# Kernel tuning notes

Hardware: AMD Instinct MI355X
Metric: run time of the kernel (lower is better)

The kernel has to match this reference:

```python
import jax, jax.numpy as jnp
import numpy as np

B, C, N = 4, 192, 4096
K = 16                      # avg degree
E = B * N * K               # 262144 edges
C_OUT = 384


def setup_inputs() -> dict:
    key = jax.random.key(0)
    k1, k2, k3, k4 = jax.random.split(key, 4)
    x = jax.random.normal(k1, (B, C, N, 1), dtype=jnp.float32)
    edge_index = jax.random.randint(k2, (2, E), 0, B * N, dtype=jnp.int64)
    # BasicConv([2C, C_OUT]): 1x1 Conv2d + bias + ReLU (norm=None)
    W = jax.random.normal(k3, (C_OUT, 2 * C), dtype=jnp.float32) * (1.0 / np.sqrt(2 * C))
    b = jax.random.normal(k4, (C_OUT,), dtype=jnp.float32) * 0.01
    return {"x": x, "edge_index": edge_index, "W": W, "b": b}


def reference(x, edge_index, W, b):
    Bs, Cs, Ns, _ = x.shape
    BN = Bs * Ns
    # (B,C,N,1) -> flattened node table (B*N, C); node id = b*N + n
    x_flat = jnp.transpose(x[..., 0], (0, 2, 1)).reshape(BN, Cs)
    x_i = x_flat[edge_index[0]]          # (E, C) gather at dst
    x_j = x_flat[edge_index[1]]          # (E, C) gather at src
    diff = x_j - x_i
    # scatter-max over dst nodes; torch_scatter fills empty segments with 0
    agg = jax.ops.segment_max(diff, edge_index[0], num_segments=BN)
    agg = jnp.where(jnp.isfinite(agg), agg, 0.0)
    x_j_out = jnp.transpose(agg.reshape(Bs, Ns, Cs), (0, 2, 1))[..., None]  # (B,C,N,1)
    # interleave channels: cat along new axis 2 then reshape -> (B, 2C, N, 1)
    cat = jnp.stack([x, x_j_out], axis=2).reshape(Bs, 2 * Cs, Ns, 1)
    # 1x1 conv == GEMM over channels, + bias + ReLU
    out = jnp.einsum('oc,bcnw->bonw', W, cat) + b[None, :, None, None]
    return jax.nn.relu(out)
```

## Files before the change

kernel.cpp:

```cpp
#include <hip/hip_runtime.h>
#include <hip/hip_bf16.h>
#include <math.h>

#define Bz    4
#define Cch   192
#define Nn    4096
#define BN    16384
#define Ecnt  262144
#define COUT  384
#define CAP   64

typedef __attribute__((ext_vector_type(8))) short short8;
typedef __attribute__((ext_vector_type(4))) float floatx4;

__device__ __forceinline__ void gload_lds16(const void* g, void* l) {
    __builtin_amdgcn_global_load_lds(
        (const __attribute__((address_space(1))) unsigned int*)g,
        (__attribute__((address_space(3))) unsigned int*)l, 16, 0, 0);
}

__device__ __forceinline__ float b2f(unsigned short u) {
    union { unsigned int i; float f; } z; z.i = ((unsigned int)u) << 16; return z.f;
}
__device__ __forceinline__ unsigned short f2b(float f) {
    __hip_bfloat16 h = __float2bfloat16(f);
    return *(unsigned short*)&h;
}

__global__ __launch_bounds__(256) void prep_kernel(
    const float* __restrict__ x, const unsigned int* __restrict__ ew,
    const float* __restrict__ W, __hip_bfloat16* __restrict__ xb,
    __hip_bfloat16* __restrict__ Wxa, __hip_bfloat16* __restrict__ Wa,
    int* __restrict__ deg, int* __restrict__ flag) {
    int bid = blockIdx.x;
    if (bid < 3072) {
        __shared__ float tile[32][33];
        int b = bid / 768;
        int r = bid - b * 768;
        int c0 = (r >> 7) * 32;
        int n0 = (r & 127) * 32;
        int tx = threadIdx.x & 31, ty = threadIdx.x >> 5;
        for (int i = ty; i < 32; i += 8)
            tile[i][tx] = x[((size_t)(b * Cch + c0 + i)) * Nn + n0 + tx];
        __syncthreads();
        for (int i = ty; i < 32; i += 8)
            xb[((size_t)(b * Nn + n0 + i)) * Cch + c0 + tx] =
                __float2bfloat16(tile[tx][i]);
    } else if (bid < 3360) {
        int i = (bid - 3072) * 256 + threadIdx.x;
        int o = i / Cch, c = i - o * Cch;
        float wx = W[o * 2 * Cch + 2 * c];
        float wa = W[o * 2 * Cch + 2 * c + 1];
        Wxa[i] = __float2bfloat16(wx - wa);
        Wa[i]  = __float2bfloat16(wa);
    } else if (bid < 3424) {
        deg[(bid - 3360) * 256 + threadIdx.x] = 0;
    } else {
        __shared__ int s;
        if (threadIdx.x == 0) s = 1;
        __syncthreads();
        if (ew[2 * threadIdx.x + 1] != 0u) atomicAnd(&s, 0);
        __syncthreads();
        if (threadIdx.x == 0) *flag = s;
    }
}

__global__ __launch_bounds__(256) void fill_kernel(
    const int* __restrict__ ew, const int* __restrict__ flag,
    int* __restrict__ deg, int* __restrict__ slots) {
    int t = blockIdx.x * 256 + threadIdx.x;
    int d0, d1, s0, s1;
    if (*flag) {
        int4 dv = *(const int4*)&ew[4 * t];
        int4 sv = *(const int4*)&ew[2 * Ecnt + 4 * t];
        d0 = dv.x; d1 = dv.z; s0 = sv.x; s1 = sv.z;
    } else {
        int2 dv = *(const int2*)&ew[2 * t];
        int2 sv = *(const int2*)&ew[Ecnt + 2 * t];
        d0 = dv.x; d1 = dv.y; s0 = sv.x; s1 = sv.y;
    }
    int p0 = atomicAdd(&deg[d0], 1); if (p0 < CAP) slots[(d0 << 6) + p0] = s0;
    int p1 = atomicAdd(&deg[d1], 1); if (p1 < CAP) slots[(d1 << 6) + p1] = s1;
}

__global__ __launch_bounds__(256) void agg_kernel(
    const int* __restrict__ deg, const int* __restrict__ slots,
    const __hip_bfloat16* __restrict__ xb, __hip_bfloat16* __restrict__ Mb) {
    int lane = threadIdx.x & 63, wave = threadIdx.x >> 6;
    int node = (blockIdx.x << 2) + wave;
    int d = deg[node]; if (d > CAP) d = CAP;
    int nbrval = 0;
    if (lane < d) nbrval = slots[(node << 6) + lane];
    const unsigned short* xbu = (const unsigned short*)xb;
    int act = lane < 48;
    int cb = lane * 4;
    float m0 = -INFINITY, m1 = -INFINITY, m2 = -INFINITY, m3 = -INFINITY;
    int k = 0;
    for (; k + 4 <= d; k += 4) {
        int s0 = __shfl(nbrval, k);
        int s1 = __shfl(nbrval, k + 1);
        int s2 = __shfl(nbrval, k + 2);
        int s3 = __shfl(nbrval, k + 3);
        if (act) {
            ushort4 v0 = *(const ushort4*)&xbu[s0 * Cch + cb];
            ushort4 v1 = *(const ushort4*)&xbu[s1 * Cch + cb];
            ushort4 v2 = *(const ushort4*)&xbu[s2 * Cch + cb];
            ushort4 v3 = *(const ushort4*)&xbu[s3 * Cch + cb];
            m0 = fmaxf(fmaxf(m0, b2f(v0.x)), fmaxf(fmaxf(b2f(v1.x), b2f(v2.x)), b2f(v3.x)));
            m1 = fmaxf(fmaxf(m1, b2f(v0.y)), fmaxf(fmaxf(b2f(v1.y), b2f(v2.y)), b2f(v3.y)));
            m2 = fmaxf(fmaxf(m2, b2f(v0.z)), fmaxf(fmaxf(b2f(v1.z), b2f(v2.z)), b2f(v3.z)));
            m3 = fmaxf(fmaxf(m3, b2f(v0.w)), fmaxf(fmaxf(b2f(v1.w), b2f(v2.w)), b2f(v3.w)));
        }
    }
    for (; k < d; k++) {
        int s = __shfl(nbrval, k);
        if (act) {
            ushort4 v = *(const ushort4*)&xbu[s * Cch + cb];
            m0 = fmaxf(m0, b2f(v.x)); m1 = fmaxf(m1, b2f(v.y));
            m2 = fmaxf(m2, b2f(v.z)); m3 = fmaxf(m3, b2f(v.w));
        }
    }
    if (act) {
        ushort4 o4;
        if (d > 0) {
            o4.x = f2b(m0); o4.y = f2b(m1); o4.z = f2b(m2); o4.w = f2b(m3);
        } else {
            o4 = *(const ushort4*)&xbu[node * Cch + cb];
        }
        *(ushort4*)&((unsigned short*)Mb)[node * Cch + cb] = o4;
    }
}

__global__ __launch_bounds__(256) void gemm_kernel(
    const __hip_bfloat16* __restrict__ Xb, const __hip_bfloat16* __restrict__ Ab,
    const __hip_bfloat16* __restrict__ Wxa, const __hip_bfloat16* __restrict__ Wa,
    const float* __restrict__ bias, float* __restrict__ out) {
    __shared__ short As[64 * 32];
    __shared__ short Bs[128 * 32];
    int t = threadIdx.x;
    int node0 = blockIdx.x * 64;
    int o0    = blockIdx.y * 128;
    int lane = t & 63, wave = t >> 6;
    int quad = lane >> 4, lrow = lane & 15;
    int wm = wave & 1, wn = wave >> 1;

    floatx4 acc[2][4] = {};
    int srow = t >> 2;
    int koff = (t & 3) * 8;

    const __hip_bfloat16* Asrc[2] = {Xb, Ab};
    const __hip_bfloat16* Bsrc[2] = {Wxa, Wa};

    for (int seg = 0; seg < 2; seg++) {
        const __hip_bfloat16* a_g = Asrc[seg] + (size_t)(node0 + srow) * Cch + koff;
        const __hip_bfloat16* b_g = Bsrc[seg] + (size_t)(o0 + srow) * Cch + koff;
        for (int kt = 0; kt < Cch; kt += 32) {
            __syncthreads();
            gload_lds16(a_g + kt,                    &As[t * 8]);
            gload_lds16(b_g + kt,                    &Bs[t * 8]);
            gload_lds16(b_g + kt + (size_t)64 * Cch, &Bs[2048 + t * 8]);
            __syncthreads();
            short8 af[2], bf[4];
#pragma unroll
            for (int i = 0; i < 2; i++)
                af[i] = *(const short8*)&As[(wm * 32 + i * 16 + lrow) * 32 + quad * 8];
#pragma unroll
            for (int j = 0; j < 4; j++)
                bf[j] = *(const short8*)&Bs[(wn * 64 + j * 16 + lrow) * 32 + quad * 8];
#pragma unroll
            for (int i = 0; i < 2; i++)
#pragma unroll
                for (int j = 0; j < 4; j++)
                    acc[i][j] = __builtin_amdgcn_mfma_f32_16x16x32_bf16(bf[j], af[i], acc[i][j], 0, 0, 0);
        }
    }

#pragma unroll
    for (int i = 0; i < 2; i++) {
        int node = node0 + wm * 32 + i * 16 + lrow;
        int b = node >> 12, n = node & 4095;
#pragma unroll
        for (int j = 0; j < 4; j++) {
            int ob = o0 + wn * 64 + j * 16 + quad * 4;
#pragma unroll
            for (int r = 0; r < 4; r++) {
                int o = ob + r;
                float v = acc[i][j][r] + bias[o];
                out[((size_t)(b * COUT + o)) * Nn + n] = fmaxf(v, 0.0f);
            }
        }
    }
}

extern "C" void kernel_launch(void* const* d_in, const int* in_sizes, int n_in,
                              void* d_out, int out_size, void* d_ws, size_t ws_size,
                              hipStream_t stream) {
    const float* x    = (const float*)d_in[0];
    const int*   ew   = (const int*)d_in[1];
    const float* W    = (const float*)d_in[2];
    const float* bias = (const float*)d_in[3];
    float* out        = (float*)d_out;

    char* ws = (char*)d_ws;
    __hip_bfloat16* xb   = (__hip_bfloat16*)ws;
    __hip_bfloat16* Mb   = (__hip_bfloat16*)(ws + 6291456);
    __hip_bfloat16* Wxa  = (__hip_bfloat16*)(ws + 12582912);
    __hip_bfloat16* Wa   = (__hip_bfloat16*)(ws + 12730368);
    int* deg   = (int*)(ws + 12877824);
    int* slots = (int*)(ws + 12943360);
    int* flag  = (int*)(ws + 17137664);

    prep_kernel<<<3425, 256, 0, stream>>>(x, (const unsigned int*)ew, W, xb, Wxa, Wa, deg, flag);
    fill_kernel<<<Ecnt / 512, 256, 0, stream>>>(ew, flag, deg, slots);
    agg_kernel<<<BN / 4, 256, 0, stream>>>(deg, slots, xb, Mb);
    gemm_kernel<<<dim3(BN / 64, COUT / 128), 256, 0, stream>>>(xb, Mb, Wxa, Wa, bias, out);
}
```

Measured before the change: 117.2 us.

## Double-buffer GEMM LDS tiles and unroll aggregation gather to 8 neighbors

The GEMM kernel now ping-pongs between two LDS buffers, issuing the next K-slab's global-to-LDS loads before computing on the current one, with one barrier per step instead of two. The aggregation kernel makes the degree wave-uniform, uses readlane instead of shuffles for neighbor indices, and processes eight neighbor rows per iteration to put more gathers in flight. The aim is to hide global load latency in both kernels, at the cost of doubled LDS use and more registers. The double-buffer relies on the barrier at the end of each step to keep the buffer being refilled safe from reads still in progress.

```diff
diff --git a/kernel.cpp b/kernel.cpp
--- a/kernel.cpp
+++ b/kernel.cpp
@@ -83,12 +83,20 @@
     int p1 = atomicAdd(&deg[d1], 1); if (p1 < CAP) slots[(d1 << 6) + p1] = s1;
 }
 
+#define RED8(mm, FLD) do {                                                    \
+    float a_ = fmaxf(fmaxf(b2f(v[0].FLD), b2f(v[1].FLD)),                     \
+                     fmaxf(b2f(v[2].FLD), b2f(v[3].FLD)));                    \
+    float b_ = fmaxf(fmaxf(b2f(v[4].FLD), b2f(v[5].FLD)),                     \
+                     fmaxf(b2f(v[6].FLD), b2f(v[7].FLD)));                    \
+    mm = fmaxf(mm, fmaxf(a_, b_)); } while (0)
+
 __global__ __launch_bounds__(256) void agg_kernel(
     const int* __restrict__ deg, const int* __restrict__ slots,
     const __hip_bfloat16* __restrict__ xb, __hip_bfloat16* __restrict__ Mb) {
     int lane = threadIdx.x & 63, wave = threadIdx.x >> 6;
     int node = (blockIdx.x << 2) + wave;
     int d = deg[node]; if (d > CAP) d = CAP;
+    d = __builtin_amdgcn_readfirstlane(d);
     int nbrval = 0;
     if (lane < d) nbrval = slots[(node << 6) + lane];
     const unsigned short* xbu = (const unsigned short*)xb;
@@ -96,24 +104,36 @@
     int cb = lane * 4;
     float m0 = -INFINITY, m1 = -INFINITY, m2 = -INFINITY, m3 = -INFINITY;
     int k = 0;
-    for (; k + 4 <= d; k += 4) {
-        int s0 = __shfl(nbrval, k);
-        int s1 = __shfl(nbrval, k + 1);
-        int s2 = __shfl(nbrval, k + 2);
-        int s3 = __shfl(nbrval, k + 3);
+    for (; k + 8 <= d; k += 8) {
+        int s[8];
+#pragma unroll
+        for (int u = 0; u < 8; u++) s[u] = __builtin_amdgcn_readlane(nbrval, k + u);
+        if (act) {
+            ushort4 v[8];
+#pragma unroll
+            for (int u = 0; u < 8; u++) v[u] = *(const ushort4*)&xbu[s[u] * Cch + cb];
+            RED8(m0, x); RED8(m1, y); RED8(m2, z); RED8(m3, w);
+        }
+    }
+    if (k + 4 <= d) {
+        int s0 = __builtin_amdgcn_readlane(nbrval, k);
+        int s1 = __builtin_amdgcn_readlane(nbrval, k + 1);
+        int s2 = __builtin_amdgcn_readlane(nbrval, k + 2);
+        int s3 = __builtin_amdgcn_readlane(nbrval, k + 3);
         if (act) {
             ushort4 v0 = *(const ushort4*)&xbu[s0 * Cch + cb];
             ushort4 v1 = *(const ushort4*)&xbu[s1 * Cch + cb];
             ushort4 v2 = *(const ushort4*)&xbu[s2 * Cch + cb];
             ushort4 v3 = *(const ushort4*)&xbu[s3 * Cch + cb];
-            m0 = fmaxf(fmaxf(m0, b2f(v0.x)), fmaxf(fmaxf(b2f(v1.x), b2f(v2.x)), b2f(v3.x)));
-            m1 = fmaxf(fmaxf(m1, b2f(v0.y)), fmaxf(fmaxf(b2f(v1.y), b2f(v2.y)), b2f(v3.y)));
-            m2 = fmaxf(fmaxf(m2, b2f(v0.z)), fmaxf(fmaxf(b2f(v1.z), b2f(v2.z)), b2f(v3.z)));
-            m3 = fmaxf(fmaxf(m3, b2f(v0.w)), fmaxf(fmaxf(b2f(v1.w), b2f(v2.w)), b2f(v3.w)));
-        }
+            m0 = fmaxf(m0, fmaxf(fmaxf(b2f(v0.x), b2f(v1.x)), fmaxf(b2f(v2.x), b2f(v3.x))));
+            m1 = fmaxf(m1, fmaxf(fmaxf(b2f(v0.y), b2f(v1.y)), fmaxf(b2f(v2.y), b2f(v3.y))));
+            m2 = fmaxf(m2, fmaxf(fmaxf(b2f(v0.z), b2f(v1.z)), fmaxf(b2f(v2.z), b2f(v3.z))));
+            m3 = fmaxf(m3, fmaxf(fmaxf(b2f(v0.w), b2f(v1.w)), fmaxf(b2f(v2.w), b2f(v3.w))));
+        }
+        k += 4;
     }
     for (; k < d; k++) {
-        int s = __shfl(nbrval, k);
+        int s = __builtin_amdgcn_readlane(nbrval, k);
         if (act) {
             ushort4 v = *(const ushort4*)&xbu[s * Cch + cb];
             m0 = fmaxf(m0, b2f(v.x)); m1 = fmaxf(m1, b2f(v.y));
@@ -135,8 +155,8 @@
     const __hip_bfloat16* __restrict__ Xb, const __hip_bfloat16* __restrict__ Ab,
     const __hip_bfloat16* __restrict__ Wxa, const __hip_bfloat16* __restrict__ Wa,
     const float* __restrict__ bias, float* __restrict__ out) {
-    __shared__ short As[64 * 32];
-    __shared__ short Bs[128 * 32];
+    __shared__ short As[2][64 * 32];
+    __shared__ short Bs[2][128 * 32];
     int t = threadIdx.x;
     int node0 = blockIdx.x * 64;
     int o0    = blockIdx.y * 128;
@@ -148,31 +168,37 @@
     int srow = t >> 2;
     int koff = (t & 3) * 8;
 
-    const __hip_bfloat16* Asrc[2] = {Xb, Ab};
-    const __hip_bfloat16* Bsrc[2] = {Wxa, Wa};
-
-    for (int seg = 0; seg < 2; seg++) {
-        const __hip_bfloat16* a_g = Asrc[seg] + (size_t)(node0 + srow) * Cch + koff;
-        const __hip_bfloat16* b_g = Bsrc[seg] + (size_t)(o0 + srow) * Cch + koff;
-        for (int kt = 0; kt < Cch; kt += 32) {
-            __syncthreads();
-            gload_lds16(a_g + kt,                    &As[t * 8]);
-            gload_lds16(b_g + kt,                    &Bs[t * 8]);
-            gload_lds16(b_g + kt + (size_t)64 * Cch, &Bs[2048 + t * 8]);
-            __syncthreads();
-            short8 af[2], bf[4];
-#pragma unroll
-            for (int i = 0; i < 2; i++)
-                af[i] = *(const short8*)&As[(wm * 32 + i * 16 + lrow) * 32 + quad * 8];
+    size_t aoff = (size_t)(node0 + srow) * Cch + koff;
+    size_t boff = (size_t)(o0 + srow) * Cch + koff;
+    const __hip_bfloat16* Ag[2] = {Xb + aoff, Ab + aoff};
+    const __hip_bfloat16* Bg[2] = {Wxa + boff, Wa + boff};
+
+    auto STAGE = [&](int s, int b) {
+        int seg = (s >= 6);
+        int kt = (seg ? s - 6 : s) * 32;
+        gload_lds16(Ag[seg] + kt, &As[b][t * 8]);
+        gload_lds16(Bg[seg] + kt, &Bs[b][t * 8]);
+        gload_lds16(Bg[seg] + (size_t)64 * Cch + kt, &Bs[b][2048 + t * 8]);
+    };
+
+    STAGE(0, 0);
+    __syncthreads();
+    for (int s = 0; s < 12; s++) {
+        int p = s & 1;
+        if (s < 11) STAGE(s + 1, p ^ 1);
+        short8 af[2], bf[4];
+#pragma unroll
+        for (int i = 0; i < 2; i++)
+            af[i] = *(const short8*)&As[p][(wm * 32 + i * 16 + lrow) * 32 + quad * 8];
+#pragma unroll
+        for (int j = 0; j < 4; j++)
+            bf[j] = *(const short8*)&Bs[p][(wn * 64 + j * 16 + lrow) * 32 + quad * 8];
+#pragma unroll
+        for (int i = 0; i < 2; i++)
 #pragma unroll
             for (int j = 0; j < 4; j++)
-                bf[j] = *(const short8*)&Bs[(wn * 64 + j * 16 + lrow) * 32 + quad * 8];
-#pragma unroll
-            for (int i = 0; i < 2; i++)
-#pragma unroll
-                for (int j = 0; j < 4; j++)
-                    acc[i][j] = __builtin_amdgcn_mfma_f32_16x16x32_bf16(bf[j], af[i], acc[i][j], 0, 0, 0);
-        }
+                acc[i][j] = __builtin_amdgcn_mfma_f32_16x16x32_bf16(bf[j], af[i], acc[i][j], 0, 0, 0);
+        __syncthreads();
     }
 
 #pragma unroll
```

After: 115.5 us. Within noise of the previous version (-1.4%).
